# Performance work log

Hardware: AMD Instinct MI355X
Metric: run time of the kernel (lower is better)

Reference implementation:

```python
import jax, jax.numpy as jnp
import numpy as np

N_NODES = 64
KS = (52, 42, 34)  # ceil(0.8*64), ceil(0.8*52), ceil(0.8*42)


def _gcn(x, A, W, b):
    # GCNConv(improved=True): self-loop fill 2.0, symmetric normalization. A[tgt, src], weighted.
    n = A.shape[0]
    Ah = A + 2.0 * jnp.eye(n, dtype=A.dtype)
    d = Ah.sum(-1)
    dis = jnp.where(d > 0, jax.lax.rsqrt(d), 0.0)
    An = dis[:, None] * Ah * dis[None, :]
    return An @ (x @ W) + b


def _augment(A):
    # GraphUNet.augment_adj: add self loops (weight 1), A2 = A1 @ A1, remove self loops
    n = A.shape[0]
    eye = jnp.eye(n, dtype=A.dtype)
    A1 = A + eye
    return (A1 @ A1) * (1.0 - eye)


def _pool(x, A, w, k):
    # TopKPooling: score = tanh(x.w/||w||), keep top-k, scale kept features by score
    s = jnp.tanh((x @ w) / jnp.linalg.norm(w))
    sv, perm = jax.lax.top_k(s, k)
    return x[perm] * sv[:, None], A[perm][:, perm], perm


def _unet(x, A, dw0, db0, dws, dbs, pws, uws, ubs, uwl, ubl):
    # GraphUNet(depth=3, sum_res=True), single graph: x [n, F2], A [n, n]
    x = jax.nn.relu(_gcn(x, A, dw0, db0))
    xs, As, perms = [x], [A], []
    for i in range(3):
        A = _augment(A)
        x, A, perm = _pool(x, A, pws[i], KS[i])
        x = jax.nn.relu(_gcn(x, A, dws[i], dbs[i]))
        if i < 2:
            xs.append(x)
            As.append(A)
        perms.append(perm)
    for i in range(3):
        j = 2 - i
        res, Aj, perm = xs[j], As[j], perms[j]
        x = res + jnp.zeros_like(res).at[perm].set(x)
        if i < 2:
            x = jax.nn.relu(_gcn(x, Aj, uws[i], ubs[i]))
        else:
            x = _gcn(x, Aj, uwl, ubl)
    return x


def _nnconv(x, src, dst, ea, mw, mb, rw, bias):
    # NNConv(aggr='mean'): per-edge MLP weight, gather-matmul-scatter-mean + root + bias
    B, E = src.shape
    fin, fout = rw.shape
    We = jax.nn.relu(ea @ mw + mb).reshape(B, E, fin, fout)  # [B,E,fin,fout]
    xs = jnp.take_along_axis(x, src[..., None], axis=1)      # [B,E,fin]
    msg = jnp.einsum('bei,beio->beo', xs, We)                # [B,E,fout]
    seg = jax.vmap(lambda m, d: jax.ops.segment_sum(m, d, num_segments=N_NODES))
    sums = seg(msg, dst)
    cnt = seg(jnp.ones(msg.shape[:2] + (1,), msg.dtype), dst)
    agg = sums / jnp.maximum(cnt, 1.0)
    return agg + x @ rw + bias


def _adj(src, dst):
    A = jnp.zeros((N_NODES, N_NODES), jnp.float32).at[dst, src].set(1.0)
    return A * (1.0 - jnp.eye(N_NODES, dtype=jnp.float32))


def _branch(x, ei, ea, mlp1, mlp2, u1, u2):
    src, dst = ei[:, 0], ei[:, 1]
    A = jax.vmap(_adj)(src, dst)
    x = jax.nn.relu(_nnconv(x, src, dst, ea, *mlp1))
    x = jax.nn.relu(jax.vmap(lambda h, a: _unet(h, a, *u1))(x, A))
    x = jax.nn.relu(_nnconv(x, src, dst, ea, *mlp2))
    x = jax.nn.relu(jax.vmap(lambda h, a: _unet(h, a, *u2))(x, A))
    return x.mean(axis=1)  # global_mean_pool (equal-sized graphs)


def setup_inputs() -> dict:
    key = jax.random.key(0)
    keys = iter(jax.random.split(key, 64))
    def nrm(shape, s=1.0):
        return jax.random.normal(next(keys), shape, jnp.float32) * s
    B, n, E, F, F2, Q, H, C = 128, 64, 512, 64, 32, 16, 256, 50
    inp = {}
    inp['x1'] = nrm((B, n, F))
    inp['ei1'] = jax.random.randint(next(keys), (B, 2, E), 0, n, jnp.int32)
    inp['ea1'] = jax.random.uniform(next(keys), (B, E, 1), jnp.float32)
    inp['jw1'] = nrm((B, Q))
    inp['x2'] = nrm((B, n, F))
    inp['ei2'] = jax.random.randint(next(keys), (B, 2, E), 0, n, jnp.int32)
    inp['ea2'] = jax.random.uniform(next(keys), (B, E, 1), jnp.float32)
    inp['jw2'] = nrm((B, Q))
    inp['m1w'] = nrm((1, F * F2), 0.1)
    inp['m1b'] = nrm((F * F2,), 0.1)
    inp['r1w'] = nrm((F, F2), 0.1)
    inp['c1b'] = nrm((F2,), 0.1)
    inp['m2w'] = nrm((1, F2 * F2), 0.1)
    inp['m2b'] = nrm((F2 * F2,), 0.1)
    inp['r2w'] = nrm((F2, F2), 0.1)
    inp['c2b'] = nrm((F2,), 0.1)
    for p in ('u1', 'u2'):
        inp[p + '_dw0'] = nrm((F2, C), 0.1)
        inp[p + '_db0'] = nrm((C,), 0.1)
        inp[p + '_dws'] = nrm((3, C, C), 0.1)
        inp[p + '_dbs'] = nrm((3, C), 0.1)
        inp[p + '_pws'] = nrm((3, C), 0.1)
        inp[p + '_uws'] = nrm((2, C, C), 0.1)
        inp[p + '_ubs'] = nrm((2, C), 0.1)
        inp[p + '_uwl'] = nrm((C, F2), 0.1)
        inp[p + '_ubl'] = nrm((F2,), 0.1)
    inp['bb_w'] = nrm(((F2 + Q) * 2, H), 0.1)
    inp['bb_b'] = nrm((H,), 0.1)
    return inp


def reference(x1, ei1, ea1, jw1, x2, ei2, ea2, jw2,
              m1w, m1b, r1w, c1b, m2w, m2b, r2w, c2b,
              u1_dw0, u1_db0, u1_dws, u1_dbs, u1_pws, u1_uws, u1_ubs, u1_uwl, u1_ubl,
              u2_dw0, u2_db0, u2_dws, u2_dbs, u2_pws, u2_uws, u2_ubs, u2_uwl, u2_ubl,
              bb_w, bb_b):
    mlp1 = (m1w, m1b, r1w, c1b)
    mlp2 = (m2w, m2b, r2w, c2b)
    u1 = (u1_dw0, u1_db0, u1_dws, u1_dbs, u1_pws, u1_uws, u1_ubs, u1_uwl, u1_ubl)
    u2 = (u2_dw0, u2_db0, u2_dws, u2_dbs, u2_pws, u2_uws, u2_ubs, u2_uwl, u2_ubl)
    r1 = _branch(x1, ei1, ea1, mlp1, mlp2, u1, u2)
    r2 = _branch(x2, ei2, ea2, mlp1, mlp2, u1, u2)
    c = jnp.concatenate([r1, jw1, r2, jw2], axis=1)  # [(F2+Q)*2]
    return jax.nn.relu(c @ bb_w + bb_b)
```

## Files before the change

### kernel.cpp

```cpp
#include <hip/hip_runtime.h>
#include <math.h>

#define UT 1024
#define XS 52
#define ASTR 65

__device__ __forceinline__ float wred16(float v) {
    v += __shfl_xor(v, 8); v += __shfl_xor(v, 4);
    v += __shfl_xor(v, 2); v += __shfl_xor(v, 1);
    return v;
}

__device__ __forceinline__ void gcn_u(int n, int cin, int cout,
    float* __restrict__ x, float* __restrict__ tmp,
    const float* __restrict__ A, float* __restrict__ Wl,
    float* __restrict__ dis,
    const float* __restrict__ Wg, const float* __restrict__ bg, bool relu)
{
    const int tid = threadIdx.x;
    const int nso = (cout + 3) >> 2;
    for (int idx = tid; idx < 51 * 52; idx += UT) {
        int r = idx / 52, c = idx - r * 52;
        float v = 0.f;
        if (r < cin && c < cout) v = Wg[r * cout + c];
        else if (r == 50 && c < cout) v = bg[c];
        Wl[idx] = v;
    }
    {
        int r = tid >> 4, l = tid & 15;
        float s = 0.f;
        if (r < n) for (int j = l; j < n; j += 16) s += A[r * ASTR + j];
        s = wred16(s);
        if (l == 0 && r < n) dis[r] = 1.0f / sqrtf(2.0f + s);
    }
    __syncthreads();
    const int items = n * nso;
    for (int it = tid; it < items; it += UT) {
        int i = it / nso, o0 = (it - i * nso) * 4;
        float a0=0,a1=0,a2=0,a3=0, b0=0,b1=0,b2=0,b3=0;
        for (int k = 0; k < cin; k += 2) {
            float4 w0 = *(const float4*)&Wl[k * 52 + o0];
            float4 w1 = *(const float4*)&Wl[(k + 1) * 52 + o0];
            float x0 = x[i * XS + k], x1 = x[i * XS + k + 1];
            a0 = fmaf(x0, w0.x, a0); a1 = fmaf(x0, w0.y, a1);
            a2 = fmaf(x0, w0.z, a2); a3 = fmaf(x0, w0.w, a3);
            b0 = fmaf(x1, w1.x, b0); b1 = fmaf(x1, w1.y, b1);
            b2 = fmaf(x1, w1.z, b2); b3 = fmaf(x1, w1.w, b3);
        }
        float d = dis[i];
        float4 t;
        t.x = (a0 + b0) * d; t.y = (a1 + b1) * d;
        t.z = (a2 + b2) * d; t.w = (a3 + b3) * d;
        *(float4*)&tmp[i * XS + o0] = t;
    }
    __syncthreads();
    for (int it = tid; it < items; it += UT) {
        int i = it / nso, o0 = (it - i * nso) * 4;
        float a0=0,a1=0,a2=0,a3=0, b0=0,b1=0,b2=0,b3=0;
        for (int j = 0; j < n; j += 2) {
            float4 t0 = *(const float4*)&tmp[j * XS + o0];
            float4 t1 = *(const float4*)&tmp[(j + 1) * XS + o0];
            float av0 = A[i * ASTR + j], av1 = A[i * ASTR + j + 1];
            a0 = fmaf(av0, t0.x, a0); a1 = fmaf(av0, t0.y, a1);
            a2 = fmaf(av0, t0.z, a2); a3 = fmaf(av0, t0.w, a3);
            b0 = fmaf(av1, t1.x, b0); b1 = fmaf(av1, t1.y, b1);
            b2 = fmaf(av1, t1.z, b2); b3 = fmaf(av1, t1.w, b3);
        }
        float4 bias = *(const float4*)&Wl[50 * 52 + o0];
        float4 s0 = *(const float4*)&tmp[i * XS + o0];
        float d = dis[i];
        float4 r;
        r.x = fmaf(d, (a0 + b0) + 2.f * s0.x, bias.x);
        r.y = fmaf(d, (a1 + b1) + 2.f * s0.y, bias.y);
        r.z = fmaf(d, (a2 + b2) + 2.f * s0.z, bias.z);
        r.w = fmaf(d, (a3 + b3) + 2.f * s0.w, bias.w);
        if (relu) {
            r.x = fmaxf(r.x, 0.f); r.y = fmaxf(r.y, 0.f);
            r.z = fmaxf(r.z, 0.f); r.w = fmaxf(r.w, 0.f);
        }
        *(float4*)&x[i * XS + o0] = r;
    }
    __syncthreads();
}

__device__ __forceinline__ void down_scores(int n, const float* __restrict__ wg,
                                            const float* __restrict__ px,
                                            float* __restrict__ scr)
{
    const int tid = threadIdx.x;
    int r = tid >> 4, l = tid & 15;
    float s = 0.f, wn = 0.f;
    for (int q = l; q < 50; q += 16) {
        float wv = wg[q];
        wn = fmaf(wv, wv, wn);
        s  = fmaf(px[r * XS + q], wv, s);
    }
    s = wred16(s); wn = wred16(wn);
    if (l == 0 && r < n) scr[r] = tanhf(s / sqrtf(wn));
}

__device__ __forceinline__ void down_rest(int n, int kk,
    float* __restrict__ px, float* __restrict__ pt_,
    float* __restrict__ pA, float* __restrict__ pF,
    float* __restrict__ scr, float* __restrict__ dis, float* __restrict__ svals,
    int* __restrict__ perm, const float* __restrict__ dw,
    const float* __restrict__ db)
{
    const int tid = threadIdx.x;
    __syncthreads();
    if (tid < 64) {
        float v = (tid < n) ? scr[tid] : -2.0f;
        int id = tid;
        for (int sz = 2; sz <= 64; sz <<= 1)
            for (int st = sz >> 1; st > 0; st >>= 1) {
                float ov = __shfl_xor(v, st);
                int oi = __shfl_xor(id, st);
                bool up = ((tid & sz) == 0);
                bool lower = ((tid & st) == 0);
                bool less = (v > ov) || (v == ov && id < oi);
                bool keep = (up == lower) ? less : !less;
                if (!keep) { v = ov; id = oi; }
            }
        if (tid < kk) { perm[tid] = id; svals[tid] = v; }
    }
    __syncthreads();
    for (int idx = tid; idx < n * 13; idx += UT) {
        int m = idx / 13, u0 = (idx - (idx / 13) * 13) * 4;
        float4 gv;
        gv.x = (u0 + 0 < kk) ? pA[m * ASTR + perm[u0 + 0]] : 0.f;
        gv.y = (u0 + 1 < kk) ? pA[m * ASTR + perm[u0 + 1]] : 0.f;
        gv.z = (u0 + 2 < kk) ? pA[m * ASTR + perm[u0 + 2]] : 0.f;
        gv.w = (u0 + 3 < kk) ? pA[m * ASTR + perm[u0 + 3]] : 0.f;
        *(float4*)&pt_[m * XS + u0] = gv;
    }
    float gx0=0, gx1=0, gx2=0, gx3=0; int gdst = -1;
    if (tid < kk * 13) {
        int t = tid / 13, q0 = (tid - t * 13) * 4;
        float sv = svals[t]; int p = perm[t];
        gx0 = px[p * XS + q0 + 0] * sv; gx1 = px[p * XS + q0 + 1] * sv;
        gx2 = px[p * XS + q0 + 2] * sv; gx3 = px[p * XS + q0 + 3] * sv;
        gdst = t * XS + q0;
    }
    __syncthreads();
    if (gdst >= 0) {
        px[gdst] = gx0; px[gdst + 1] = gx1; px[gdst + 2] = gx2; px[gdst + 3] = gx3;
    }
    int nst = (kk + 3) >> 2;
    for (int it = tid; it < kk * nst; it += UT) {
        int t = it / nst, u0 = (it - t * nst) * 4;
        int p = perm[t];
        float a0=0,a1=0,a2=0,a3=0, c0=0,c1=0,c2=0,c3=0;
        for (int m = 0; m < n; m += 2) {
            float4 g0 = *(const float4*)&pt_[m * XS + u0];
            float4 g1 = *(const float4*)&pt_[(m + 1) * XS + u0];
            float q0v = pA[p * ASTR + m], q1v = pA[p * ASTR + m + 1];
            a0 = fmaf(q0v, g0.x, a0); a1 = fmaf(q0v, g0.y, a1);
            a2 = fmaf(q0v, g0.z, a2); a3 = fmaf(q0v, g0.w, a3);
            c0 = fmaf(q1v, g1.x, c0); c1 = fmaf(q1v, g1.y, c1);
            c2 = fmaf(q1v, g1.z, c2); c3 = fmaf(q1v, g1.w, c3);
        }
        float4 gg = *(const float4*)&pt_[p * XS + u0];
        float v;
        v = (a0 + c0) + 2.f * gg.x; pF[t * ASTR + u0 + 0] = (u0 + 0 == t) ? 0.f : v;
        v = (a1 + c1) + 2.f * gg.y; pF[t * ASTR + u0 + 1] = (u0 + 1 == t) ? 0.f : v;
        v = (a2 + c2) + 2.f * gg.z; pF[t * ASTR + u0 + 2] = (u0 + 2 == t) ? 0.f : v;
        v = (a3 + c3) + 2.f * gg.w; pF[t * ASTR + u0 + 3] = (u0 + 3 == t) ? 0.f : v;
    }
    __syncthreads();
    gcn_u(kk, 50, 50, px, pt_, pF, pA, dis, dw, db, true);
}

__global__ __launch_bounds__(UT)
void unet_kernel(const float* __restrict__ xin, const float* __restrict__ wsA,
                 const float* __restrict__ dw0, const float* __restrict__ db0,
                 const float* __restrict__ dws, const float* __restrict__ dbs,
                 const float* __restrict__ pws,
                 const float* __restrict__ uws, const float* __restrict__ ubs,
                 const float* __restrict__ uwl, const float* __restrict__ ubl,
                 float* __restrict__ ws_xs, float* __restrict__ ws_As,
                 float* __restrict__ outp, int mean_mode)
{
    const int g = blockIdx.x, tid = threadIdx.x;
    __shared__ __align__(16) float Aa[64 * ASTR];
    __shared__ __align__(16) float Ab[64 * ASTR];
    __shared__ __align__(16) float x0c[64 * XS];
    __shared__ __align__(16) float x1c[64 * XS];
    __shared__ float scr[64];
    __shared__ float dis[64];
    __shared__ float svals[64];
    __shared__ int   permL[192];

    float *pA = Aa, *pF = Ab, *px = x0c, *pt_ = x1c;
    float* xs_g = ws_xs + (size_t)g * 9984;
    float* as_g = ws_As + (size_t)g * 6144;
    const float* wsAg = wsA + (size_t)g * 4160;
    const int nsz[4] = {64, 52, 42, 34};

    {
        const float* xg = xin + (size_t)g * 2048;
        for (int idx = tid; idx < 512; idx += UT) {
            int i = idx >> 3, o0 = (idx & 7) * 4;
            *(float4*)&px[i * XS + o0] = *(const float4*)&xg[i * 32 + o0];
        }
        for (int idx = tid; idx < 4160; idx += UT) pA[idx] = wsAg[idx];
    }
    __syncthreads();

    gcn_u(64, 32, 50, px, pt_, pA, pF, dis, dw0, db0, true);

    for (int lvl = 0; lvl < 3; lvl++) {
        int n = nsz[lvl], kk = nsz[lvl + 1];
        down_scores(n, pws + lvl * 50, px, scr);
        {
            float* xd = xs_g + lvl * 3328;
            for (int idx = tid; idx < 3328; idx += UT) xd[idx] = px[idx];
            if (lvl == 1) for (int idx = tid; idx < 3380; idx += UT) as_g[idx] = pA[idx];
            if (lvl == 2) for (int idx = tid; idx < 2730; idx += UT) as_g[3380 + idx] = pA[idx];
        }
        down_rest(n, kk, px, pt_, pA, pF, scr, dis, svals, permL + lvl * 64,
                  dws + lvl * 2500, dbs + lvl * 50);
        { float* t = pA; pA = pF; pF = t; }
    }

    for (int i2 = 0; i2 < 3; i2++) {
        int j = 2 - i2;
        int kc = nsz[j + 1];
        {
            const float* resg = xs_g + j * 3328;
            for (int idx = tid; idx < 3328; idx += UT) pt_[idx] = resg[idx];
            if (j == 0) {
                for (int idx = tid; idx < 4160; idx += UT) pF[idx] = wsAg[idx];
            } else if (j == 1) {
                for (int idx = tid; idx < 3380; idx += UT) pF[idx] = as_g[idx];
            } else {
                for (int idx = tid; idx < 2730; idx += UT) pF[idx] = as_g[3380 + idx];
            }
        }
        __syncthreads();
        const int* perm = permL + j * 64;
        for (int it = tid; it < kc * 13; it += UT) {
            int t = it / 13, q0 = (it - t * 13) * 4;
            int p = perm[t];
            pt_[p*XS+q0+0] += px[t*XS+q0+0]; pt_[p*XS+q0+1] += px[t*XS+q0+1];
            pt_[p*XS+q0+2] += px[t*XS+q0+2]; pt_[p*XS+q0+3] += px[t*XS+q0+3];
        }
        __syncthreads();
        if (i2 < 2)
            gcn_u(nsz[j], 50, 50, pt_, px, pF, pA, dis, uws + i2 * 2500, ubs + i2 * 50, true);
        else
            gcn_u(64, 50, 32, pt_, px, pF, pA, dis, uwl, ubl, false);
        { float* t2 = px; px = pt_; pt_ = t2; }
        { float* t2 = pA; pA = pF; pF = t2; }
    }

    if (mean_mode) {
        int r = tid >> 4, l = tid & 15;
        if (r < 32) {
            float s = 0.f;
            for (int i = l; i < 64; i += 16) s += fmaxf(px[i * XS + r], 0.f);
            s = wred16(s);
            if (l == 0) outp[(size_t)g * 32 + r] = s * (1.0f / 64.0f);
        }
    } else {
        float* og = outp + (size_t)g * 2048;
        for (int idx = tid; idx < 512; idx += UT) {
            int i = idx >> 3, o0 = (idx & 7) * 4;
            float4 vv = *(const float4*)&px[i * XS + o0];
            vv.x = fmaxf(vv.x, 0.f); vv.y = fmaxf(vv.y, 0.f);
            vv.z = fmaxf(vv.z, 0.f); vv.w = fmaxf(vv.w, 0.f);
            *(float4*)&og[i * 32 + o0] = vv;
        }
    }
}

template<int FIN>
__device__ __forceinline__ void nnconv_core(
    const float* __restrict__ xl, float* __restrict__ rwl,
    float* __restrict__ sums,
    const int* __restrict__ srcl, const int* __restrict__ dstl,
    const float* __restrict__ eal, const float* __restrict__ cnt,
    const float* __restrict__ mw, const float* __restrict__ mb,
    const float* __restrict__ bias, float* __restrict__ xout_g)
{
    const int tid = threadIdx.x;
    constexpr int ICN = FIN / 16;
    constexpr int EPT = 512 / (UT / (32 * ICN));
    const int o = tid & 31, ic = (tid >> 5) & (ICN - 1), er = tid / (32 * ICN);
    float mwr[16], mbr[16];
    #pragma unroll
    for (int z = 0; z < 16; z++) {
        mwr[z] = mw[(ic * 16 + z) * 32 + o];
        mbr[z] = mb[(ic * 16 + z) * 32 + o];
    }
    for (int e = er * EPT; e < er * EPT + EPT; e++) {
        int s = srcl[e]; int d = dstl[e]; float av = eal[e];
        float ac0 = 0.f, ac1 = 0.f, ac2 = 0.f, ac3 = 0.f;
        #pragma unroll
        for (int zb = 0; zb < 16; zb += 4) {
            float4 xv = *(const float4*)&xl[s * FIN + ic * 16 + zb];
            ac0 = fmaf(xv.x, fmaxf(fmaf(av, mwr[zb + 0], mbr[zb + 0]), 0.f), ac0);
            ac1 = fmaf(xv.y, fmaxf(fmaf(av, mwr[zb + 1], mbr[zb + 1]), 0.f), ac1);
            ac2 = fmaf(xv.z, fmaxf(fmaf(av, mwr[zb + 2], mbr[zb + 2]), 0.f), ac2);
            ac3 = fmaf(xv.w, fmaxf(fmaf(av, mwr[zb + 3], mbr[zb + 3]), 0.f), ac3);
        }
        float acc = (ac0 + ac1) + (ac2 + ac3);
        acc += __shfl_down(acc, 32);
        if ((tid & 32) == 0) atomicAdd(&sums[d * 32 + o], acc);
    }
    __syncthreads();
    {
        int nn = tid >> 4, o0 = (tid & 15) * 2;
        float a0 = 0.f, a1 = 0.f, b0 = 0.f, b1 = 0.f;
        for (int i = 0; i < FIN; i += 2) {
            float xv0 = xl[nn * FIN + i], xv1 = xl[nn * FIN + i + 1];
            float2 w0 = *(const float2*)&rwl[i * 32 + o0];
            float2 w1 = *(const float2*)&rwl[(i + 1) * 32 + o0];
            a0 = fmaf(xv0, w0.x, a0); a1 = fmaf(xv0, w0.y, a1);
            b0 = fmaf(xv1, w1.x, b0); b1 = fmaf(xv1, w1.y, b1);
        }
        float inv = 1.0f / fmaxf(cnt[nn], 1.f);
        float2 sv = *(const float2*)&sums[nn * 32 + o0];
        xout_g[nn * 32 + o0]     = fmaxf(fmaf(sv.x, inv, (a0 + b0) + bias[o0]),     0.f);
        xout_g[nn * 32 + o0 + 1] = fmaxf(fmaf(sv.y, inv, (a1 + b1) + bias[o0 + 1]), 0.f);
    }
}

__global__ __launch_bounds__(UT)
void nnconv1_kernel(const float* __restrict__ x1, const float* __restrict__ x2,
                    const int* __restrict__ ei1, const int* __restrict__ ei2,
                    const float* __restrict__ ea1, const float* __restrict__ ea2,
                    const float* __restrict__ mw, const float* __restrict__ mb,
                    const float* __restrict__ rw, const float* __restrict__ bias,
                    float* __restrict__ wsA, float* __restrict__ xout)
{
    const int g = blockIdx.x, tid = threadIdx.x;
    __shared__ __align__(16) float xl[4096];
    __shared__ __align__(16) float rwl[2048];
    __shared__ __align__(16) float sums[2048];
    __shared__ __align__(16) float Al[4160];
    __shared__ int   srcl[512];
    __shared__ int   dstl[512];
    __shared__ float eal[512];
    __shared__ float cnt[64];

    const float* xg; const int* eig; const float* eag;
    if (g < 128) {
        xg = x1 + (size_t)g * 4096; eig = ei1 + (size_t)g * 1024; eag = ea1 + (size_t)g * 512;
    } else {
        int h = g - 128;
        xg = x2 + (size_t)h * 4096; eig = ei2 + (size_t)h * 1024; eag = ea2 + (size_t)h * 512;
    }
    for (int i = tid; i < 4096; i += UT) xl[i] = xg[i];
    for (int i = tid; i < 2048; i += UT) { rwl[i] = rw[i]; sums[i] = 0.f; }
    for (int e = tid; e < 512; e += UT) {
        srcl[e] = eig[e]; dstl[e] = eig[512 + e]; eal[e] = eag[e];
    }
    for (int i = tid; i < 4160; i += UT) Al[i] = 0.f;
    if (tid < 64) cnt[tid] = 0.f;
    __syncthreads();
    for (int e = tid; e < 512; e += UT) Al[dstl[e] * ASTR + srcl[e]] = 1.f;
    __syncthreads();
    if (tid < 64) Al[tid * ASTR + tid] = 0.f;
    for (int e = tid; e < 512; e += UT) atomicAdd(&cnt[dstl[e]], 1.f);
    __syncthreads();
    for (int i = tid; i < 4160; i += UT) wsA[(size_t)g * 4160 + i] = Al[i];

    nnconv_core<64>(xl, rwl, sums, srcl, dstl, eal, cnt, mw, mb, bias,
                    xout + (size_t)g * 2048);
}

__global__ __launch_bounds__(UT)
void nnconv2_kernel(const float* __restrict__ xin,
                    const int* __restrict__ ei1, const int* __restrict__ ei2,
                    const float* __restrict__ ea1, const float* __restrict__ ea2,
                    const float* __restrict__ mw, const float* __restrict__ mb,
                    const float* __restrict__ rw, const float* __restrict__ bias,
                    float* __restrict__ xout)
{
    const int g = blockIdx.x, tid = threadIdx.x;
    __shared__ __align__(16) float xl[2048];
    __shared__ __align__(16) float rwl[1024];
    __shared__ __align__(16) float sums[2048];
    __shared__ int   srcl[512];
    __shared__ int   dstl[512];
    __shared__ float eal[512];
    __shared__ float cnt[64];

    const int* eig; const float* eag;
    if (g < 128) { eig = ei1 + (size_t)g * 1024; eag = ea1 + (size_t)g * 512; }
    else { int h = g - 128; eig = ei2 + (size_t)h * 1024; eag = ea2 + (size_t)h * 512; }

    const float* xg = xin + (size_t)g * 2048;
    for (int i = tid; i < 2048; i += UT) { xl[i] = xg[i]; sums[i] = 0.f; }
    for (int i = tid; i < 1024; i += UT) rwl[i] = rw[i];
    for (int e = tid; e < 512; e += UT) {
        srcl[e] = eig[e]; dstl[e] = eig[512 + e]; eal[e] = eag[e];
    }
    if (tid < 64) cnt[tid] = 0.f;
    __syncthreads();
    for (int e = tid; e < 512; e += UT) atomicAdd(&cnt[dstl[e]], 1.f);
    __syncthreads();

    nnconv_core<32>(xl, rwl, sums, srcl, dstl, eal, cnt, mw, mb, bias,
                    xout + (size_t)g * 2048);
}

__global__ __launch_bounds__(256)
void head_kernel(const float* __restrict__ r,
                 const float* __restrict__ jw1, const float* __restrict__ jw2,
                 const float* __restrict__ bw, const float* __restrict__ bb,
                 float* __restrict__ out)
{
    const int b = blockIdx.x, h = threadIdx.x;
    float acc = bb[h];
    const float* r1 = r + (size_t)b * 32;
    const float* r2 = r + (size_t)(128 + b) * 32;
    #pragma unroll
    for (int q = 0; q < 32; q++) acc += r1[q] * bw[q * 256 + h];
    #pragma unroll
    for (int q = 0; q < 16; q++) acc += jw1[b * 16 + q] * bw[(32 + q) * 256 + h];
    #pragma unroll
    for (int q = 0; q < 32; q++) acc += r2[q] * bw[(48 + q) * 256 + h];
    #pragma unroll
    for (int q = 0; q < 16; q++) acc += jw2[b * 16 + q] * bw[(80 + q) * 256 + h];
    out[(size_t)b * 256 + h] = fmaxf(acc, 0.f);
}

extern "C" void kernel_launch(void* const* d_in, const int* in_sizes, int n_in,
                              void* d_out, int out_size, void* d_ws, size_t ws_size,
                              hipStream_t stream)
{
    const float* x1  = (const float*)d_in[0];
    const int*   ei1 = (const int*)  d_in[1];
    const float* ea1 = (const float*)d_in[2];
    const float* jw1 = (const float*)d_in[3];
    const float* x2  = (const float*)d_in[4];
    const int*   ei2 = (const int*)  d_in[5];
    const float* ea2 = (const float*)d_in[6];
    const float* jw2 = (const float*)d_in[7];
    const float* m1w = (const float*)d_in[8];
    const float* m1b = (const float*)d_in[9];
    const float* r1w = (const float*)d_in[10];
    const float* c1b = (const float*)d_in[11];
    const float* m2w = (const float*)d_in[12];
    const float* m2b = (const float*)d_in[13];
    const float* r2w = (const float*)d_in[14];
    const float* c2b = (const float*)d_in[15];
    const float* u1p[9]; for (int i = 0; i < 9; i++) u1p[i] = (const float*)d_in[16 + i];
    const float* u2p[9]; for (int i = 0; i < 9; i++) u2p[i] = (const float*)d_in[25 + i];
    const float* bbw = (const float*)d_in[34];
    const float* bbb = (const float*)d_in[35];

    char* ws = (char*)d_ws;
    size_t off = 0;
    float* wsA  = (float*)(ws + off); off += 256ull * 4160 * 4;
    float* xc1  = (float*)(ws + off); off += 256ull * 2048 * 4;
    float* xu1  = (float*)(ws + off); off += 256ull * 2048 * 4;
    float* xc2  = (float*)(ws + off); off += 256ull * 2048 * 4;
    float* rr   = (float*)(ws + off); off += 256ull * 32 * 4;
    float* wxs  = (float*)(ws + off); off += 256ull * 9984 * 4;
    float* wAs  = (float*)(ws + off); off += 256ull * 6144 * 4;
    (void)ws_size; (void)in_sizes; (void)n_in; (void)out_size;

    nnconv1_kernel<<<256, UT, 0, stream>>>(x1, x2, ei1, ei2, ea1, ea2,
                                           m1w, m1b, r1w, c1b, wsA, xc1);
    unet_kernel<<<256, UT, 0, stream>>>(xc1, wsA,
        u1p[0], u1p[1], u1p[2], u1p[3], u1p[4], u1p[5], u1p[6], u1p[7], u1p[8],
        wxs, wAs, xu1, 0);
    nnconv2_kernel<<<256, UT, 0, stream>>>(xu1, ei1, ei2, ea1, ea2,
                                           m2w, m2b, r2w, c2b, xc2);
    unet_kernel<<<256, UT, 0, stream>>>(xc2, wsA,
        u2p[0], u2p[1], u2p[2], u2p[3], u2p[4], u2p[5], u2p[6], u2p[7], u2p[8],
        wxs, wAs, rr, 1);
    head_kernel<<<128, 256, 0, stream>>>(rr, jw1, jw2, bbw, bbb, (float*)d_out);
}
```

Baseline: 356.6 us.

## Use CSR sparse GCN at full-graph level and sort edges by source for NNConv

Builds a CSR of the original adjacency in nnconv1 and uses it for the first and last GCN in the UNet instead of a dense 64x64 aggregation, which also drops the dense adjacency reload for the final up-level. Edges are counting-sorted by source so NNConv can keep the gathered source feature row in registers across consecutive edges with the same source. The sorted edge lists are written to workspace and reused by nnconv2, adding extra scans and workspace traffic to nnconv1. The sparse path assumes binary adjacency with no duplicate edges, consistent with how the dense matrix was built.

Measured after the change: 337.2 us. 1.06x faster.

```diff
diff --git a/kernel.cpp b/kernel.cpp
--- a/kernel.cpp
+++ b/kernel.cpp
@@ -79,6 +79,70 @@
             r.z = fmaxf(r.z, 0.f); r.w = fmaxf(r.w, 0.f);
         }
         *(float4*)&x[i * XS + o0] = r;
+    }
+    __syncthreads();
+}
+
+__device__ __forceinline__ void gcn_sparse(int cin, int cout,
+    float* __restrict__ x, float* __restrict__ tmp,
+    const int* __restrict__ csrOff, const int* __restrict__ csrCol,
+    float* __restrict__ dis0, float* __restrict__ Wl,
+    const float* __restrict__ Wg, const float* __restrict__ bg, bool relu)
+{
+    const int tid = threadIdx.x;
+    const int nso = (cout + 3) >> 2;
+    for (int idx = tid; idx < 51 * 52; idx += UT) {
+        int r = idx / 52, c = idx - r * 52;
+        float v = 0.f;
+        if (r < cin && c < cout) v = Wg[r * cout + c];
+        else if (r == 50 && c < cout) v = bg[c];
+        Wl[idx] = v;
+    }
+    if (tid < 64)
+        dis0[tid] = 1.0f / sqrtf(2.0f + (float)(csrOff[tid + 1] - csrOff[tid]));
+    __syncthreads();
+    const int items = 64 * nso;
+    if (tid < items) {
+        int i = tid / nso, o0 = (tid - i * nso) * 4;
+        float a0=0,a1=0,a2=0,a3=0, b0=0,b1=0,b2=0,b3=0;
+        for (int k = 0; k < cin; k += 2) {
+            float4 w0 = *(const float4*)&Wl[k * 52 + o0];
+            float4 w1 = *(const float4*)&Wl[(k + 1) * 52 + o0];
+            float x0 = x[i * XS + k], x1 = x[i * XS + k + 1];
+            a0 = fmaf(x0, w0.x, a0); a1 = fmaf(x0, w0.y, a1);
+            a2 = fmaf(x0, w0.z, a2); a3 = fmaf(x0, w0.w, a3);
+            b0 = fmaf(x1, w1.x, b0); b1 = fmaf(x1, w1.y, b1);
+            b2 = fmaf(x1, w1.z, b2); b3 = fmaf(x1, w1.w, b3);
+        }
+        float d = dis0[i];
+        float4 t;
+        t.x = (a0 + b0) * d; t.y = (a1 + b1) * d;
+        t.z = (a2 + b2) * d; t.w = (a3 + b3) * d;
+        *(float4*)&tmp[i * XS + o0] = t;
+    }
+    __syncthreads();
+    if (tid < items) {
+        int i = tid / nso, o0 = (tid - i * nso) * 4;
+        int base = csrOff[i], end = csrOff[i + 1];
+        float a0 = 0.f, a1 = 0.f, a2 = 0.f, a3 = 0.f;
+        for (int p = base; p < end; p++) {
+            int j = csrCol[p];
+            float4 t = *(const float4*)&tmp[j * XS + o0];
+            a0 += t.x; a1 += t.y; a2 += t.z; a3 += t.w;
+        }
+        float4 bias = *(const float4*)&Wl[50 * 52 + o0];
+        float4 s0 = *(const float4*)&tmp[i * XS + o0];
+        float d = dis0[i];
+        float4 r;
+        r.x = fmaf(d, a0 + 2.f * s0.x, bias.x);
+        r.y = fmaf(d, a1 + 2.f * s0.y, bias.y);
+        r.z = fmaf(d, a2 + 2.f * s0.z, bias.z);
+        r.w = fmaf(d, a3 + 2.f * s0.w, bias.w);
+        if (relu) {
+            r.x = fmaxf(r.x, 0.f); r.y = fmaxf(r.y, 0.f);
+            r.z = fmaxf(r.z, 0.f); r.w = fmaxf(r.w, 0.f);
+        }
+        *(float4*)&x[tid / nso * XS + o0] = r;
     }
     __syncthreads();
 }
@@ -172,6 +236,7 @@
 
 __global__ __launch_bounds__(UT)
 void unet_kernel(const float* __restrict__ xin, const float* __restrict__ wsA,
+                 const int* __restrict__ wsCsrO, const int* __restrict__ wsCsrC,
                  const float* __restrict__ dw0, const float* __restrict__ db0,
                  const float* __restrict__ dws, const float* __restrict__ dbs,
                  const float* __restrict__ pws,
@@ -187,8 +252,11 @@
     __shared__ __align__(16) float x1c[64 * XS];
     __shared__ float scr[64];
     __shared__ float dis[64];
+    __shared__ float dis0[64];
     __shared__ float svals[64];
     __shared__ int   permL[192];
+    __shared__ int   csrOffL[65];
+    __shared__ int   csrColL[512];
 
     float *pA = Aa, *pF = Ab, *px = x0c, *pt_ = x1c;
     float* xs_g = ws_xs + (size_t)g * 9984;
@@ -203,10 +271,12 @@
             *(float4*)&px[i * XS + o0] = *(const float4*)&xg[i * 32 + o0];
         }
         for (int idx = tid; idx < 4160; idx += UT) pA[idx] = wsAg[idx];
-    }
-    __syncthreads();
-
-    gcn_u(64, 32, 50, px, pt_, pA, pF, dis, dw0, db0, true);
+        if (tid < 65) csrOffL[tid] = wsCsrO[(size_t)g * 66 + tid];
+        if (tid >= 128 && tid < 640) csrColL[tid - 128] = wsCsrC[(size_t)g * 512 + tid - 128];
+    }
+    __syncthreads();
+
+    gcn_sparse(32, 50, px, pt_, csrOffL, csrColL, dis0, pF, dw0, db0, true);
 
     for (int lvl = 0; lvl < 3; lvl++) {
         int n = nsz[lvl], kk = nsz[lvl + 1];
@@ -228,11 +298,9 @@
         {
             const float* resg = xs_g + j * 3328;
             for (int idx = tid; idx < 3328; idx += UT) pt_[idx] = resg[idx];
-            if (j == 0) {
-                for (int idx = tid; idx < 4160; idx += UT) pF[idx] = wsAg[idx];
-            } else if (j == 1) {
+            if (j == 1) {
                 for (int idx = tid; idx < 3380; idx += UT) pF[idx] = as_g[idx];
-            } else {
+            } else if (j == 2) {
                 for (int idx = tid; idx < 2730; idx += UT) pF[idx] = as_g[3380 + idx];
             }
         }
@@ -248,7 +316,7 @@
         if (i2 < 2)
             gcn_u(nsz[j], 50, 50, pt_, px, pF, pA, dis, uws + i2 * 2500, ubs + i2 * 50, true);
         else
-            gcn_u(64, 50, 32, pt_, px, pF, pA, dis, uwl, ubl, false);
+            gcn_sparse(50, 32, pt_, px, csrOffL, csrColL, dis0, pF, uwl, ubl, false);
         { float* t2 = px; px = pt_; pt_ = t2; }
         { float* t2 = pA; pA = pF; pF = t2; }
     }
@@ -275,10 +343,10 @@
 
 template<int FIN>
 __device__ __forceinline__ void nnconv_core(
-    const float* __restrict__ xl, float* __restrict__ rwl,
+    const float* __restrict__ xl, const float* __restrict__ rwl,
     float* __restrict__ sums,
-    const int* __restrict__ srcl, const int* __restrict__ dstl,
-    const float* __restrict__ eal, const float* __restrict__ cnt,
+    const int* __restrict__ sSrcL, const int* __restrict__ sDstL,
+    const float* __restrict__ sEaL, const float* __restrict__ cnt,
     const float* __restrict__ mw, const float* __restrict__ mb,
     const float* __restrict__ bias, float* __restrict__ xout_g)
 {
@@ -292,16 +360,25 @@
         mwr[z] = mw[(ic * 16 + z) * 32 + o];
         mbr[z] = mb[(ic * 16 + z) * 32 + o];
     }
+    float xc[16];
+    int sprev = -1;
     for (int e = er * EPT; e < er * EPT + EPT; e++) {
-        int s = srcl[e]; int d = dstl[e]; float av = eal[e];
+        int s = sSrcL[e];
+        if (s != sprev) {
+            sprev = s;
+            *(float4*)&xc[0]  = *(const float4*)&xl[s * FIN + ic * 16 + 0];
+            *(float4*)&xc[4]  = *(const float4*)&xl[s * FIN + ic * 16 + 4];
+            *(float4*)&xc[8]  = *(const float4*)&xl[s * FIN + ic * 16 + 8];
+            *(float4*)&xc[12] = *(const float4*)&xl[s * FIN + ic * 16 + 12];
+        }
+        float av = sEaL[e]; int d = sDstL[e];
         float ac0 = 0.f, ac1 = 0.f, ac2 = 0.f, ac3 = 0.f;
         #pragma unroll
         for (int zb = 0; zb < 16; zb += 4) {
-            float4 xv = *(const float4*)&xl[s * FIN + ic * 16 + zb];
-            ac0 = fmaf(xv.x, fmaxf(fmaf(av, mwr[zb + 0], mbr[zb + 0]), 0.f), ac0);
-            ac1 = fmaf(xv.y, fmaxf(fmaf(av, mwr[zb + 1], mbr[zb + 1]), 0.f), ac1);
-            ac2 = fmaf(xv.z, fmaxf(fmaf(av, mwr[zb + 2], mbr[zb + 2]), 0.f), ac2);
-            ac3 = fmaf(xv.w, fmaxf(fmaf(av, mwr[zb + 3], mbr[zb + 3]), 0.f), ac3);
+            ac0 = fmaf(xc[zb + 0], fmaxf(fmaf(av, mwr[zb + 0], mbr[zb + 0]), 0.f), ac0);
+            ac1 = fmaf(xc[zb + 1], fmaxf(fmaf(av, mwr[zb + 1], mbr[zb + 1]), 0.f), ac1);
+            ac2 = fmaf(xc[zb + 2], fmaxf(fmaf(av, mwr[zb + 2], mbr[zb + 2]), 0.f), ac2);
+            ac3 = fmaf(xc[zb + 3], fmaxf(fmaf(av, mwr[zb + 3], mbr[zb + 3]), 0.f), ac3);
         }
         float acc = (ac0 + ac1) + (ac2 + ac3);
         acc += __shfl_down(acc, 32);
@@ -331,7 +408,9 @@
                     const float* __restrict__ ea1, const float* __restrict__ ea2,
                     const float* __restrict__ mw, const float* __restrict__ mb,
                     const float* __restrict__ rw, const float* __restrict__ bias,
-                    float* __restrict__ wsA, float* __restrict__ xout)
+                    float* __restrict__ wsA, int* __restrict__ wsSrt,
+                    int* __restrict__ wsCsrO, int* __restrict__ wsCsrC,
+                    float* __restrict__ xout)
 {
     const int g = blockIdx.x, tid = threadIdx.x;
     __shared__ __align__(16) float xl[4096];
@@ -341,7 +420,14 @@
     __shared__ int   srcl[512];
     __shared__ int   dstl[512];
     __shared__ float eal[512];
+    __shared__ int   sSrcL[512];
+    __shared__ int   sDstL[512];
+    __shared__ float sEaL[512];
     __shared__ float cnt[64];
+    __shared__ int   sTot[64];
+    __shared__ int   sOff[65];
+    __shared__ int   rowc[64];
+    __shared__ int   csrOffL[65];
 
     const float* xg; const int* eig; const float* eag;
     if (g < 128) {
@@ -350,29 +436,86 @@
         int h = g - 128;
         xg = x2 + (size_t)h * 4096; eig = ei2 + (size_t)h * 1024; eag = ea2 + (size_t)h * 512;
     }
+    int* chunkCnt = (int*)sums;
+
     for (int i = tid; i < 4096; i += UT) xl[i] = xg[i];
-    for (int i = tid; i < 2048; i += UT) { rwl[i] = rw[i]; sums[i] = 0.f; }
     for (int e = tid; e < 512; e += UT) {
         srcl[e] = eig[e]; dstl[e] = eig[512 + e]; eal[e] = eag[e];
     }
     for (int i = tid; i < 4160; i += UT) Al[i] = 0.f;
+    for (int i = tid; i < 1024; i += UT) chunkCnt[i] = 0;
     if (tid < 64) cnt[tid] = 0.f;
     __syncthreads();
     for (int e = tid; e < 512; e += UT) Al[dstl[e] * ASTR + srcl[e]] = 1.f;
-    __syncthreads();
-    if (tid < 64) Al[tid * ASTR + tid] = 0.f;
+    for (int e = tid; e < 512; e += UT) atomicAdd(&chunkCnt[(e >> 5) * 64 + srcl[e]], 1);
+    __syncthreads();
+    if (tid < 64) {
+        Al[tid * ASTR + tid] = 0.f;
+        int run = 0;
+        for (int c = 0; c < 16; c++) {
+            int t = chunkCnt[c * 64 + tid];
+            chunkCnt[c * 64 + tid] = run; run += t;
+        }
+        sTot[tid] = run;
+    }
+    __syncthreads();
+    if (tid < 64) {
+        int v = sTot[tid]; int x = v;
+        #pragma unroll
+        for (int d = 1; d < 64; d <<= 1) {
+            int y = __shfl_up(x, d);
+            if (tid >= d) x += y;
+        }
+        sOff[tid] = x - v;
+        if (tid == 63) sOff[64] = x;
+    }
+    if (tid >= 64 && tid < 128) {
+        int i = tid - 64; int c = 0;
+        for (int j = 0; j < 64; j++) c += (Al[i * ASTR + j] != 0.f) ? 1 : 0;
+        rowc[i] = c;
+    }
     for (int e = tid; e < 512; e += UT) atomicAdd(&cnt[dstl[e]], 1.f);
-    __syncthreads();
+    for (int i = tid; i < 2048; i += UT) rwl[i] = rw[i];
     for (int i = tid; i < 4160; i += UT) wsA[(size_t)g * 4160 + i] = Al[i];
-
-    nnconv_core<64>(xl, rwl, sums, srcl, dstl, eal, cnt, mw, mb, bias,
+    __syncthreads();
+    if (tid < 64) {
+        int v = rowc[tid]; int x = v;
+        #pragma unroll
+        for (int d = 1; d < 64; d <<= 1) {
+            int y = __shfl_up(x, d);
+            if (tid >= d) x += y;
+        }
+        csrOffL[tid] = x - v;
+        if (tid == 63) csrOffL[64] = x;
+    }
+    for (int e = tid; e < 512; e += UT) {
+        int s = srcl[e]; int c = e >> 5; int lr = 0;
+        for (int e2 = (c << 5); e2 < e; e2++) lr += (srcl[e2] == s) ? 1 : 0;
+        int pos = sOff[s] + chunkCnt[c * 64 + s] + lr;
+        sSrcL[pos] = s; sDstL[pos] = dstl[e]; sEaL[pos] = eal[e];
+    }
+    __syncthreads();
+    if (tid < 64) {
+        int p = csrOffL[tid];
+        for (int j = 0; j < 64; j++)
+            if (Al[tid * ASTR + j] != 0.f) wsCsrC[(size_t)g * 512 + (p++)] = j;
+    }
+    if (tid >= 64 && tid < 129) wsCsrO[(size_t)g * 66 + (tid - 64)] = csrOffL[tid - 64];
+    for (int e = tid; e < 512; e += UT) {
+        wsSrt[(size_t)g * 1536 + e] = sSrcL[e];
+        wsSrt[(size_t)g * 1536 + 512 + e] = sDstL[e];
+        ((float*)wsSrt)[(size_t)g * 1536 + 1024 + e] = sEaL[e];
+    }
+    for (int i = tid; i < 2048; i += UT) sums[i] = 0.f;
+    __syncthreads();
+
+    nnconv_core<64>(xl, rwl, sums, sSrcL, sDstL, sEaL, cnt, mw, mb, bias,
                     xout + (size_t)g * 2048);
 }
 
 __global__ __launch_bounds__(UT)
 void nnconv2_kernel(const float* __restrict__ xin,
-                    const int* __restrict__ ei1, const int* __restrict__ ei2,
-                    const float* __restrict__ ea1, const float* __restrict__ ea2,
+                    const int* __restrict__ wsSrt,
                     const float* __restrict__ mw, const float* __restrict__ mb,
                     const float* __restrict__ rw, const float* __restrict__ bias,
                     float* __restrict__ xout)
@@ -381,27 +524,25 @@
     __shared__ __align__(16) float xl[2048];
     __shared__ __align__(16) float rwl[1024];
     __shared__ __align__(16) float sums[2048];
-    __shared__ int   srcl[512];
-    __shared__ int   dstl[512];
-    __shared__ float eal[512];
+    __shared__ int   sSrcL[512];
+    __shared__ int   sDstL[512];
+    __shared__ float sEaL[512];
     __shared__ float cnt[64];
-
-    const int* eig; const float* eag;
-    if (g < 128) { eig = ei1 + (size_t)g * 1024; eag = ea1 + (size_t)g * 512; }
-    else { int h = g - 128; eig = ei2 + (size_t)h * 1024; eag = ea2 + (size_t)h * 512; }
 
     const float* xg = xin + (size_t)g * 2048;
     for (int i = tid; i < 2048; i += UT) { xl[i] = xg[i]; sums[i] = 0.f; }
     for (int i = tid; i < 1024; i += UT) rwl[i] = rw[i];
     for (int e = tid; e < 512; e += UT) {
-        srcl[e] = eig[e]; dstl[e] = eig[512 + e]; eal[e] = eag[e];
+        sSrcL[e] = wsSrt[(size_t)g * 1536 + e];
+        sDstL[e] = wsSrt[(size_t)g * 1536 + 512 + e];
+        sEaL[e]  = ((const float*)wsSrt)[(size_t)g * 1536 + 1024 + e];
     }
     if (tid < 64) cnt[tid] = 0.f;
     __syncthreads();
-    for (int e = tid; e < 512; e += UT) atomicAdd(&cnt[dstl[e]], 1.f);
-    __syncthreads();
-
-    nnconv_core<32>(xl, rwl, sums, srcl, dstl, eal, cnt, mw, mb, bias,
+    for (int e = tid; e < 512; e += UT) atomicAdd(&cnt[sDstL[e]], 1.f);
+    __syncthreads();
+
+    nnconv_core<32>(xl, rwl, sums, sSrcL, sDstL, sEaL, cnt, mw, mb, bias,
                     xout + (size_t)g * 2048);
 }
 
@@ -460,16 +601,19 @@
     float* rr   = (float*)(ws + off); off += 256ull * 32 * 4;
     float* wxs  = (float*)(ws + off); off += 256ull * 9984 * 4;
     float* wAs  = (float*)(ws + off); off += 256ull * 6144 * 4;
+    int*   wSrt = (int*)  (ws + off); off += 256ull * 1536 * 4;
+    int*   wCsO = (int*)  (ws + off); off += 256ull * 66 * 4;
+    int*   wCsC = (int*)  (ws + off); off += 256ull * 512 * 4;
     (void)ws_size; (void)in_sizes; (void)n_in; (void)out_size;
 
     nnconv1_kernel<<<256, UT, 0, stream>>>(x1, x2, ei1, ei2, ea1, ea2,
-                                           m1w, m1b, r1w, c1b, wsA, xc1);
-    unet_kernel<<<256, UT, 0, stream>>>(xc1, wsA,
+                                           m1w, m1b, r1w, c1b,
+                                           wsA, wSrt, wCsO, wCsC, xc1);
+    unet_kernel<<<256, UT, 0, stream>>>(xc1, wsA, wCsO, wCsC,
         u1p[0], u1p[1], u1p[2], u1p[3], u1p[4], u1p[5], u1p[6], u1p[7], u1p[8],
         wxs, wAs, xu1, 0);
-    nnconv2_kernel<<<256, UT, 0, stream>>>(xu1, ei1, ei2, ea1, ea2,
-                                           m2w, m2b, r2w, c2b, xc2);
-    unet_kernel<<<256, UT, 0, stream>>>(xc2, wsA,
+    nnconv2_kernel<<<256, UT, 0, stream>>>(xu1, wSrt, m2w, m2b, r2w, c2b, xc2);
+    unet_kernel<<<256, UT, 0, stream>>>(xc2, wsA, wCsO, wCsC,
         u2p[0], u2p[1], u2p[2], u2p[3], u2p[4], u2p[5], u2p[6], u2p[7], u2p[8],
         wxs, wAs, rr, 1);
     head_kernel<<<128, 256, 0, stream>>>(rr, jw1, jw2, bbw, bbb, (float*)d_out);
```
